# Performance work log

Measured on AMD Instinct MI355X. Metric: run time of the kernel, lower is better.

The kernel has to match this reference:

```python
import jax, jax.numpy as jnp
import numpy as np

B, C, P, NG, NCLS, HID, N, IMG = 2, 256, 7, 2, 81, 1024, 512, 800
STRIDES = [4, 8, 16, 32]
SCALE = 56.0  # roi_map_level_scale


def _roi_align(feat, rois, pooled, scale, ng):
    """torchvision-legacy (aligned=False) ROI Align. feat [B,C,H,W], rois [N,5]."""
    Bf, Cf, H, W = feat.shape
    ft = jnp.transpose(feat, (0, 2, 3, 1))  # [B,H,W,C]
    b = rois[:, 0].astype(jnp.int32)
    x1, y1, x2, y2 = (rois[:, i] * scale for i in (1, 2, 3, 4))
    rw = jnp.maximum(x2 - x1, 1.0)
    rh = jnp.maximum(y2 - y1, 1.0)
    # sample grid per output bin: ng points per axis, centered in sub-bins
    g = (jnp.arange(pooled)[:, None] + (jnp.arange(ng)[None, :] + 0.5) / ng).reshape(-1)  # [P*ng]
    ys = y1[:, None] + g[None, :] * (rh / pooled)[:, None]  # [N,S]
    xs = x1[:, None] + g[None, :] * (rw / pooled)[:, None]

    def axis(coord, size):
        valid = (coord >= -1.0) & (coord <= size)
        c = jnp.clip(coord, 0.0, size - 1)
        lo = jnp.floor(c).astype(jnp.int32)
        hi = jnp.minimum(lo + 1, size - 1)
        return valid, lo, hi, c - lo

    vy, ylo, yhi, fy = axis(ys, H)
    vx, xlo, xhi, fx = axis(xs, W)
    bb = b[:, None, None]

    def gather(yi, xi):
        return ft[bb, yi[:, :, None], xi[:, None, :], :]  # [N,S,S,C]

    wy = fy[:, :, None, None]
    wx = fx[:, None, :, None]
    val = ((1 - wy) * (1 - wx) * gather(ylo, xlo) + (1 - wy) * wx * gather(ylo, xhi)
           + wy * (1 - wx) * gather(yhi, xlo) + wy * wx * gather(yhi, xhi))
    val = jnp.where((vy[:, :, None] & vx[:, None, :])[..., None], val, 0.0)
    val = val.reshape(-1, pooled, ng, pooled, ng, Cf).mean(axis=(2, 4))  # [N,P,P,C]
    return jnp.transpose(val, (0, 3, 1, 2))  # [N,C,P,P]


def setup_inputs() -> dict:
    key = jax.random.key(0)
    ks = jax.random.split(key, 16)
    feats = {}
    for i, s in enumerate(STRIDES):
        hw = IMG // s
        feats[f"p{i+2}"] = jax.random.normal(ks[i], (B, C, hw, hw), jnp.float32)
    # realistic proposals: batch idx + boxes with sizes 16..512 px
    bidx = jax.random.randint(ks[4], (N,), 0, B).astype(jnp.float32)
    sw = 2.0 ** jax.random.uniform(ks[5], (N,), minval=4.0, maxval=9.0)
    sh = 2.0 ** jax.random.uniform(ks[6], (N,), minval=4.0, maxval=9.0)
    x1 = jax.random.uniform(ks[7], (N,)) * (IMG - sw)
    y1 = jax.random.uniform(ks[8], (N,)) * (IMG - sh)
    rois = jnp.stack([bidx, x1, y1, x1 + sw - 1, y1 + sh - 1], axis=1)
    D = C * P * P
    inp = dict(feats, rois=rois,
               w1=0.01 * jax.random.normal(ks[9], (HID, D), jnp.float32),
               b1=jnp.zeros((HID,), jnp.float32),
               w2=0.01 * jax.random.normal(ks[10], (HID, HID), jnp.float32),
               b2=jnp.zeros((HID,), jnp.float32),
               w_cls=0.01 * jax.random.normal(ks[11], (NCLS, HID), jnp.float32),
               b_cls=jnp.zeros((NCLS,), jnp.float32),
               w_reg=0.001 * jax.random.normal(ks[12], (NCLS * 4, HID), jnp.float32),
               b_reg=jnp.zeros((NCLS * 4,), jnp.float32))
    return inp


def reference(p2, p3, p4, p5, rois, w1, b1, w2, b2, w_cls, b_cls, w_reg, b_reg):
    feats = [p2, p3, p4, p5]
    # FPN level assignment (same math as torch: log2(sqrt(hw)/scale + 1e-6), floor, clamp)
    rh = rois[:, 4] - rois[:, 2] + 1
    rw = rois[:, 3] - rois[:, 1] + 1
    levels = jnp.clip(jnp.floor(jnp.log2(jnp.sqrt(rh * rw) / SCALE + 1e-6)), 0, 3).astype(jnp.int32)
    # dispatch: compute each ROI on its assigned level (masked combine == gather/sort-scatter)
    pooled = jnp.zeros((rois.shape[0], C, P, P), rois.dtype)
    for l, feat in enumerate(feats):
        pl = _roi_align(feat, rois, P, 1.0 / STRIDES[l], NG)
        pooled = pooled + jnp.where((levels == l)[:, None, None, None], pl, 0.0)
    x = pooled.reshape(pooled.shape[0], -1)  # [N, C*P*P]
    x = jax.nn.relu(x @ w1.T + b1)
    x = jax.nn.relu(x @ w2.T + b2)
    x_cls = x @ w_cls.T + b_cls
    x_reg = x @ w_reg.T + b_reg  # TEST mode, not class-agnostic: no gather
    cls_probs = jax.nn.softmax(x_cls, axis=1)
    rois_out = rois.reshape(B, -1, 5)
    cls_probs = cls_probs.reshape(B, rois_out.shape[1], -1)
    bbox_preds = x_reg.reshape(B, rois_out.shape[1], -1)
    return rois_out, cls_probs, bbox_preds
```

## Files before the change

### kernel.cpp

```cpp
#include <hip/hip_runtime.h>
#include <hip/hip_bf16.h>
#include <math.h>

#define NROI   512
#define CCH    256
#define POOLP  7
#define DDIM   12544
#define HIDN   1024
#define NCLS   81
#define NREG   324
#define NHEAD  512
#define OUT_ROIS   2560
#define OUT_CLS    (512*81)

typedef __attribute__((ext_vector_type(4))) float f32x4;
typedef __attribute__((ext_vector_type(8))) short bf16x8;

static __device__ __forceinline__ unsigned short f2bf(float x) {
    __hip_bfloat16 h = __float2bfloat16(x);
    return *reinterpret_cast<unsigned short*>(&h);
}
static __device__ __forceinline__ float bf2f(unsigned short u) {
    unsigned int b = ((unsigned int)u) << 16;
    return *reinterpret_cast<float*>(&b);
}

#define PP_B0 10
#define PP_B1 (PP_B0 + 1280)
#define PP_B2 (PP_B1 + 1024)
#define PP_B3 (PP_B2 + 1024)
#define PP_B4 (PP_B3 + 1024)
#define PP_B5 (PP_B4 + 13296)
__global__ __launch_bounds__(256) void preprocess_k(
        const float* __restrict__ rois, const float* __restrict__ w1,
        const float* __restrict__ w2, const float* __restrict__ wc,
        const float* __restrict__ wr,
        const float* __restrict__ p2, const float* __restrict__ p3,
        const float* __restrict__ p4, const float* __restrict__ p5,
        float* __restrict__ out, float* __restrict__ accz,
        unsigned short* __restrict__ w1b, unsigned short* __restrict__ w2b,
        unsigned short* __restrict__ whd,
        unsigned short* __restrict__ f0, unsigned short* __restrict__ f1,
        unsigned short* __restrict__ f2, unsigned short* __restrict__ f3) {
    __shared__ unsigned short sm[49 * 258];
    int bid = blockIdx.x, t = threadIdx.x;

    if (bid < PP_B0) {
        int i = bid * 256 + t;
        if (i < OUT_ROIS) out[i] = rois[i];
    } else if (bid < PP_B1) {
        int i = (bid - PP_B0) * 256 + t;
        ((float4*)accz)[i] = make_float4(0.f, 0.f, 0.f, 0.f);
    } else if (bid < PP_B2) {
        int i = (bid - PP_B1) * 256 + t;
        float4 v = ((const float4*)w2)[i];
        ushort4 o;
        o.x = f2bf(v.x); o.y = f2bf(v.y); o.z = f2bf(v.z); o.w = f2bf(v.w);
        ((ushort4*)w2b)[i] = o;
    } else if (bid < PP_B3) {
        int i2 = (bid - PP_B2) * 256 + t;
        int r = i2 >> 9, c = (i2 & 511) << 1;
        float v0, v1;
        if (r < NCLS)             { v0 = wc[r * HIDN + c]; v1 = wc[r * HIDN + c + 1]; }
        else if (r < NCLS + NREG) { v0 = wr[(r - NCLS) * HIDN + c]; v1 = wr[(r - NCLS) * HIDN + c + 1]; }
        else                      { v0 = 0.f; v1 = 0.f; }
        ((unsigned int*)whd)[i2] = (unsigned int)f2bf(v0) | ((unsigned int)f2bf(v1) << 16);
    } else if (bid < PP_B4) {
        int n = bid - PP_B3;
        const float* src = w1 + (size_t)n * DDIM;
        for (int k = t; k < DDIM; k += 256) {
            int c = k / 49;
            int s = k - c * 49;
            sm[s * 258 + c] = f2bf(src[k]);
        }
        __syncthreads();
        unsigned int* dst = (unsigned int*)(w1b + (size_t)n * DDIM);
        for (int j2 = t; j2 < DDIM / 2; j2 += 256) {
            int s = j2 >> 7, c2 = (j2 & 127) << 1;
            dst[j2] = sm[s * 258 + c2] | ((unsigned int)sm[s * 258 + c2 + 1] << 16);
        }
    } else {
        int j  = bid - PP_B4;
        int xb = j % 1662;
        int q  = j / 1662;
        int c0 = (q & 3) * 64;
        int b  = q >> 2;
        const float* in; unsigned short* op; int S, base;
        if (xb < 1250)      { in = p2; op = f0; S = 40000; base = 0; }
        else if (xb < 1563) { in = p3; op = f1; S = 10000; base = 1250; }
        else if (xb < 1642) { in = p4; op = f2; S = 2500;  base = 1563; }
        else                { in = p5; op = f3; S = 625;   base = 1642; }
        int s0 = (xb - base) * 32;
        {
            int sL = t & 31, cq = t >> 5;
            const float* src = in + ((size_t)b * CCH + c0 + cq * 8) * S + s0 + sL;
            bool ok = (s0 + sL) < S;
#pragma unroll
            for (int jj = 0; jj < 8; jj++)
                sm[sL * 66 + cq * 8 + jj] = ok ? f2bf(src[(size_t)jj * S]) : (unsigned short)0;
        }
        __syncthreads();
        {
            int c2 = t & 31, sq = t >> 5;
#pragma unroll
            for (int i = 0; i < 4; i++) {
                int s = sq * 4 + i;
                if (s0 + s < S) {
                    unsigned int v = sm[s * 66 + c2 * 2]
                                   | ((unsigned int)sm[s * 66 + c2 * 2 + 1] << 16);
                    ((unsigned int*)(op + ((size_t)b * S + s0 + s) * CCH + c0))[c2] = v;
                }
            }
        }
    }
}

__global__ __launch_bounds__(256) void roi_align_k(const unsigned short* __restrict__ f0,
                                                   const unsigned short* __restrict__ f1,
                                                   const unsigned short* __restrict__ f2,
                                                   const unsigned short* __restrict__ f3,
                                                   const float* __restrict__ rois,
                                                   unsigned short* __restrict__ xpool) {
    __shared__ float s_f[16];
    __shared__ int   s_lo[16], s_hi[16], s_v[16];

    int py = blockIdx.x, r = blockIdx.y, t = threadIdx.x;

    float r0  = rois[r * 5 + 0];
    float rx1 = rois[r * 5 + 1], ry1 = rois[r * 5 + 2];
    float rx2 = rois[r * 5 + 3], ry2 = rois[r * 5 + 4];
    int b = (int)r0;

    float aw = rx2 - rx1 + 1.f, ah = ry2 - ry1 + 1.f;
    float lvf = floorf(log2f(sqrtf(ah * aw) / 56.f + 1e-6f));
    int lv = (int)fminf(fmaxf(lvf, 0.f), 3.f);

    const unsigned short* F = (lv == 0) ? f0 : (lv == 1) ? f1 : (lv == 2) ? f2 : f3;
    int HW      = (lv == 0) ? 200 : (lv == 1) ? 100 : (lv == 2) ? 50 : 25;
    float scale = (lv == 0) ? 0.25f : (lv == 1) ? 0.125f : (lv == 2) ? 0.0625f : 0.03125f;

    float x1 = rx1 * scale, yy1 = ry1 * scale;
    float x2 = rx2 * scale, yy2 = ry2 * scale;
    float rw = fmaxf(x2 - x1, 1.f), rh = fmaxf(yy2 - yy1, 1.f);

    if (t < 16) {
        bool isY = t < 2;
        float coord;
        if (isY) {
            float g = (float)py + ((float)t + 0.5f) * 0.5f;
            coord = yy1 + g * (rh * (1.f / 7.f));
        } else {
            int j = t - 2;
            float g = (float)(j >> 1) + ((float)(j & 1) + 0.5f) * 0.5f;
            coord = x1 + g * (rw * (1.f / 7.f));
        }
        int vld = (coord >= -1.f && coord <= (float)HW) ? 1 : 0;
        float c = fminf(fmaxf(coord, 0.f), (float)(HW - 1));
        int lo  = (int)floorf(c);
        int hi  = min(lo + 1, HW - 1);
        s_v[t] = vld; s_lo[t] = lo; s_hi[t] = hi; s_f[t] = c - (float)lo;
    }
    __syncthreads();

    const unsigned short* Fb = F + ((size_t)b * HW * HW) * CCH + t;
    size_t obase = (size_t)r * DDIM + py * 7 * 256 + t;

    for (int px = 0; px < POOLP; px++) {
        float acc = 0.f;
#pragma unroll
        for (int s = 0; s < 4; s++) {
            int iy = s >> 1;
            int ix = px * 2 + (s & 1);
            int vy = s_v[iy], vx = s_v[2 + ix];
            if (vy & vx) {
                float fy = s_f[iy], fx = s_f[2 + ix];
                int ylo = s_lo[iy], yhi = s_hi[iy];
                int xlo = s_lo[2 + ix], xhi = s_hi[2 + ix];
                float v00 = bf2f(Fb[((size_t)ylo * HW + xlo) * CCH]);
                float v01 = bf2f(Fb[((size_t)ylo * HW + xhi) * CCH]);
                float v10 = bf2f(Fb[((size_t)yhi * HW + xlo) * CCH]);
                float v11 = bf2f(Fb[((size_t)yhi * HW + xhi) * CCH]);
                acc += (1.f - fy) * ((1.f - fx) * v00 + fx * v01)
                     + fy * ((1.f - fx) * v10 + fx * v11);
            }
        }
        xpool[obase + px * 256] = f2bf(acc * 0.25f);
    }
}

__global__ __launch_bounds__(256) void roi_align_nchw_k(const float* __restrict__ f0,
                                                        const float* __restrict__ f1,
                                                        const float* __restrict__ f2,
                                                        const float* __restrict__ f3,
                                                        const float* __restrict__ rois,
                                                        unsigned short* __restrict__ xpool) {
    __shared__ float s_f[16];
    __shared__ int   s_lo[16], s_hi[16], s_v[16];
    int py = blockIdx.x, r = blockIdx.y, t = threadIdx.x;
    float r0  = rois[r * 5 + 0];
    float rx1 = rois[r * 5 + 1], ry1 = rois[r * 5 + 2];
    float rx2 = rois[r * 5 + 3], ry2 = rois[r * 5 + 4];
    int b = (int)r0;
    float aw = rx2 - rx1 + 1.f, ah = ry2 - ry1 + 1.f;
    float lvf = floorf(log2f(sqrtf(ah * aw) / 56.f + 1e-6f));
    int lv = (int)fminf(fmaxf(lvf, 0.f), 3.f);
    const float* F = (lv == 0) ? f0 : (lv == 1) ? f1 : (lv == 2) ? f2 : f3;
    int HW      = (lv == 0) ? 200 : (lv == 1) ? 100 : (lv == 2) ? 50 : 25;
    float scale = (lv == 0) ? 0.25f : (lv == 1) ? 0.125f : (lv == 2) ? 0.0625f : 0.03125f;
    float x1 = rx1 * scale, yy1 = ry1 * scale;
    float x2 = rx2 * scale, yy2 = ry2 * scale;
    float rw = fmaxf(x2 - x1, 1.f), rh = fmaxf(yy2 - yy1, 1.f);
    if (t < 16) {
        bool isY = t < 2;
        float coord;
        if (isY) {
            float g = (float)py + ((float)t + 0.5f) * 0.5f;
            coord = yy1 + g * (rh * (1.f / 7.f));
        } else {
            int j = t - 2;
            float g = (float)(j >> 1) + ((float)(j & 1) + 0.5f) * 0.5f;
            coord = x1 + g * (rw * (1.f / 7.f));
        }
        int vld = (coord >= -1.f && coord <= (float)HW) ? 1 : 0;
        float c = fminf(fmaxf(coord, 0.f), (float)(HW - 1));
        int lo  = (int)floorf(c);
        int hi  = min(lo + 1, HW - 1);
        s_v[t] = vld; s_lo[t] = lo; s_hi[t] = hi; s_f[t] = c - (float)lo;
    }
    __syncthreads();
    const float* Fb = F + ((size_t)b * CCH + t) * HW * HW;
    size_t obase = (size_t)r * DDIM + py * 7 * 256 + t;
    for (int px = 0; px < POOLP; px++) {
        float acc = 0.f;
#pragma unroll
        for (int s = 0; s < 4; s++) {
            int iy = s >> 1, ix = px * 2 + (s & 1);
            int vy = s_v[iy], vx = s_v[2 + ix];
            if (vy & vx) {
                float fy = s_f[iy], fx = s_f[2 + ix];
                int ylo = s_lo[iy], yhi = s_hi[iy];
                int xlo = s_lo[2 + ix], xhi = s_hi[2 + ix];
                float v00 = Fb[(size_t)ylo * HW + xlo];
                float v01 = Fb[(size_t)ylo * HW + xhi];
                float v10 = Fb[(size_t)yhi * HW + xlo];
                float v11 = Fb[(size_t)yhi * HW + xhi];
                acc += (1.f - fy) * ((1.f - fx) * v00 + fx * v01)
                     + fy * ((1.f - fx) * v10 + fx * v11);
            }
        }
        xpool[obase + px * 256] = f2bf(acc * 0.25f);
    }
}

__global__ __launch_bounds__(256) void gemm_bf16_k(const unsigned short* __restrict__ A,
                                                   const unsigned short* __restrict__ W,
                                                   float* __restrict__ Cacc,
                                                   int M, int N, int K, int kchunk) {
    __shared__ __align__(16) unsigned short As[2][8][64][8];
    __shared__ __align__(16) unsigned short Ws[2][8][64][8];

    int t = threadIdx.x;
    int lane = t & 63, wid = t >> 6;
    int m0 = blockIdx.y * 64, n0 = blockIdx.x * 64;
    int k0 = blockIdx.z * kchunk;
    int wm = (wid >> 1) * 32, wn = (wid & 1) * 32;
    int fr = lane & 15, kg = lane >> 4;
    int nsteps = kchunk >> 6;

    f32x4 acc[2][2] = {};

    const unsigned short* Arow = A + (size_t)(m0 + lane) * K;
    const unsigned short* Wrow = W + (size_t)(n0 + lane) * K;

    auto stage = [&](int buf, int kb) {
#pragma unroll
        for (int i = 0; i < 2; i++) {
            int c = wid * 2 + i;
            __builtin_amdgcn_global_load_lds(
                (const __attribute__((address_space(1))) void*)(Arow + kb + c * 8),
                (__attribute__((address_space(3))) void*)(&As[buf][c][0][0]), 16, 0, 0);
            __builtin_amdgcn_global_load_lds(
                (const __attribute__((address_space(1))) void*)(Wrow + kb + c * 8),
                (__attribute__((address_space(3))) void*)(&Ws[buf][c][0][0]), 16, 0, 0);
        }
    };

    stage(0, k0);
    __syncthreads();
    int cur = 0;
    for (int tt = 0; tt < nsteps; ++tt) {
        if (tt + 1 < nsteps) stage(cur ^ 1, k0 + (tt + 1) * 64);
#pragma unroll
        for (int h = 0; h < 2; h++) {
            bf16x8 a0 = *(const bf16x8*)(&As[cur][h * 4 + kg][wm + fr][0]);
            bf16x8 a1 = *(const bf16x8*)(&As[cur][h * 4 + kg][wm + 16 + fr][0]);
            bf16x8 b0 = *(const bf16x8*)(&Ws[cur][h * 4 + kg][wn + fr][0]);
            bf16x8 b1 = *(const bf16x8*)(&Ws[cur][h * 4 + kg][wn + 16 + fr][0]);
            acc[0][0] = __builtin_amdgcn_mfma_f32_16x16x32_bf16(a0, b0, acc[0][0], 0, 0, 0);
            acc[0][1] = __builtin_amdgcn_mfma_f32_16x16x32_bf16(a0, b1, acc[0][1], 0, 0, 0);
            acc[1][0] = __builtin_amdgcn_mfma_f32_16x16x32_bf16(a1, b0, acc[1][0], 0, 0, 0);
            acc[1][1] = __builtin_amdgcn_mfma_f32_16x16x32_bf16(a1, b1, acc[1][1], 0, 0, 0);
        }
        __syncthreads();
        cur ^= 1;
    }

    int row = m0 + wm + (lane >> 4) * 4;
    int col = n0 + wn + fr;
#pragma unroll
    for (int fm = 0; fm < 2; fm++)
#pragma unroll
        for (int fn = 0; fn < 2; fn++)
#pragma unroll
            for (int r = 0; r < 4; r++)
                atomicAdd(&Cacc[(size_t)(row + fm * 16 + r) * N + col + fn * 16],
                          acc[fm][fn][r]);
}

__global__ __launch_bounds__(256) void gemm128_bf16_k(const unsigned short* __restrict__ A,
                                                      const unsigned short* __restrict__ W,
                                                      float* __restrict__ Cacc,
                                                      int M, int N, int K, int kchunk) {
    __shared__ __align__(16) unsigned short As[2][8][128][8];
    __shared__ __align__(16) unsigned short Ws[2][8][128][8];

    int lin  = blockIdx.x;
    int nb   = (lin & 7) * 56 + (lin >> 3);
    int tile = nb / 14, bz = nb - tile * 14;
    int bx = tile & 7, by = tile >> 3;

    int t = threadIdx.x;
    int lane = t & 63, wid = t >> 6;
    int m0 = by * 128, n0 = bx * 128;
    int k0 = bz * kchunk;
    int wm = (wid >> 1) * 64, wn = (wid & 1) * 64;
    int fr = lane & 15, kg = lane >> 4;
    int nsteps = kchunk >> 6;

    f32x4 acc[4][4] = {};

    auto stage = [&](int buf, int kb) {
#pragma unroll
        for (int i = 0; i < 4; i++) {
            int c   = wid * 4 + i;
            int kgc = c >> 1;
            int r0w = (c & 1) * 64;
            __builtin_amdgcn_global_load_lds(
                (const __attribute__((address_space(1))) void*)
                    (A + (size_t)(m0 + r0w + lane) * K + kb + kgc * 8),
                (__attribute__((address_space(3))) void*)(&As[buf][kgc][r0w][0]), 16, 0, 0);
            __builtin_amdgcn_global_load_lds(
                (const __attribute__((address_space(1))) void*)
                    (W + (size_t)(n0 + r0w + lane) * K + kb + kgc * 8),
                (__attribute__((address_space(3))) void*)(&Ws[buf][kgc][r0w][0]), 16, 0, 0);
        }
    };

    stage(0, k0);
    __syncthreads();
    int cur = 0;
    for (int tt = 0; tt < nsteps; ++tt) {
        if (tt + 1 < nsteps) stage(cur ^ 1, k0 + (tt + 1) * 64);
#pragma unroll
        for (int h = 0; h < 2; h++) {
            bf16x8 av[4], bv[4];
#pragma unroll
            for (int f = 0; f < 4; f++) {
                av[f] = *(const bf16x8*)(&As[cur][h * 4 + kg][wm + f * 16 + fr][0]);
                bv[f] = *(const bf16x8*)(&Ws[cur][h * 4 + kg][wn + f * 16 + fr][0]);
            }
#pragma unroll
            for (int fm = 0; fm < 4; fm++)
#pragma unroll
                for (int fn = 0; fn < 4; fn++)
                    acc[fm][fn] = __builtin_amdgcn_mfma_f32_16x16x32_bf16(
                        av[fm], bv[fn], acc[fm][fn], 0, 0, 0);
        }
        __syncthreads();
        cur ^= 1;
    }

    int row = m0 + wm + (lane >> 4) * 4;
    int col = n0 + wn + fr;
#pragma unroll
    for (int fm = 0; fm < 4; fm++)
#pragma unroll
        for (int fn = 0; fn < 4; fn++)
#pragma unroll
            for (int r = 0; r < 4; r++)
                atomicAdd(&Cacc[(size_t)(row + fm * 16 + r) * N + col + fn * 16],
                          acc[fm][fn][r]);
}

__global__ __launch_bounds__(256) void fc_ep_k(const float* __restrict__ acc,
                                               const float* __restrict__ bias,
                                               unsigned short* __restrict__ dst, int MN) {
    int i = blockIdx.x * 256 + threadIdx.x;
    if (i >= MN) return;
    float s = fmaxf(acc[i] + bias[i & (HIDN - 1)], 0.f);
    dst[i] = f2bf(s);
}

__global__ void head_ep_k(const float* __restrict__ hf,
                          const float* __restrict__ bc,
                          const float* __restrict__ br,
                          float* __restrict__ out) {
    int r = blockIdx.x, l = threadIdx.x;
    const float* row = hf + (size_t)r * NHEAD;

    float* reg = out + OUT_ROIS + OUT_CLS + (size_t)r * NREG;
    for (int j = l; j < NREG; j += 64) reg[j] = row[NCLS + j] + br[j];

    float v0 = row[l] + bc[l];
    float v1 = (l + 64 < NCLS) ? row[l + 64] + bc[l + 64] : -INFINITY;
    float m = fmaxf(v0, v1);
#pragma unroll
    for (int o = 32; o; o >>= 1) m = fmaxf(m, __shfl_xor(m, o));
    float e0 = __expf(v0 - m);
    float e1 = (l + 64 < NCLS) ? __expf(v1 - m) : 0.f;
    float s = e0 + e1;
#pragma unroll
    for (int o = 32; o; o >>= 1) s += __shfl_xor(s, o);
    float inv = 1.f / s;
    float* cls = out + OUT_ROIS + (size_t)r * NCLS;
    cls[l] = e0 * inv;
    if (l + 64 < NCLS) cls[l + 64] = e1 * inv;
}

extern "C" void kernel_launch(void* const* d_in, const int* in_sizes, int n_in,
                              void* d_out, int out_size, void* d_ws, size_t ws_size,
                              hipStream_t stream) {
    const float* p2   = (const float*)d_in[0];
    const float* p3   = (const float*)d_in[1];
    const float* p4   = (const float*)d_in[2];
    const float* p5   = (const float*)d_in[3];
    const float* rois = (const float*)d_in[4];
    const float* w1   = (const float*)d_in[5];
    const float* b1   = (const float*)d_in[6];
    const float* w2   = (const float*)d_in[7];
    const float* b2   = (const float*)d_in[8];
    const float* wc   = (const float*)d_in[9];
    const float* bc   = (const float*)d_in[10];
    const float* wr   = (const float*)d_in[11];
    const float* br   = (const float*)d_in[12];

    float* out = (float*)d_out;

    const int KS1 = 14;

    char* p = (char*)d_ws;
    auto alloc = [&](size_t bytes) { char* r = p; p += (bytes + 255) & ~(size_t)255; return r; };
    unsigned short* xpool = (unsigned short*)alloc((size_t)NROI * DDIM * 2);
    unsigned short* y1b   = (unsigned short*)alloc((size_t)NROI * HIDN * 2);
    unsigned short* y2b   = (unsigned short*)alloc((size_t)NROI * HIDN * 2);
    unsigned short* w1b   = (unsigned short*)alloc((size_t)HIDN * DDIM * 2);
    unsigned short* w2b   = (unsigned short*)alloc((size_t)HIDN * HIDN * 2);
    unsigned short* whd   = (unsigned short*)alloc((size_t)NHEAD * HIDN * 2);
    float*          accz  = (float*)alloc((size_t)(NROI * HIDN * 2 + NROI * NHEAD) * 4);
    unsigned short* ft0 = (unsigned short*)alloc((size_t)2 * 40000 * CCH * 2);
    unsigned short* ft1 = (unsigned short*)alloc((size_t)2 * 10000 * CCH * 2);
    unsigned short* ft2 = (unsigned short*)alloc((size_t)2 * 2500 * CCH * 2);
    unsigned short* ft3 = (unsigned short*)alloc((size_t)2 * 625 * CCH * 2);
    bool nhwc = (size_t)(p - (char*)d_ws) <= ws_size;

    float* y1f = accz;
    float* y2f = accz + (size_t)NROI * HIDN;
    float* hf  = accz + (size_t)NROI * HIDN * 2;

    preprocess_k<<<nhwc ? PP_B5 : PP_B4, 256, 0, stream>>>(
        rois, w1, w2, wc, wr, p2, p3, p4, p5,
        out, accz, w1b, w2b, whd, ft0, ft1, ft2, ft3);

    if (nhwc) {
        roi_align_k<<<dim3(POOLP, NROI), 256, 0, stream>>>(ft0, ft1, ft2, ft3, rois, xpool);
    } else {
        roi_align_nchw_k<<<dim3(POOLP, NROI), 256, 0, stream>>>(p2, p3, p4, p5, rois, xpool);
    }

    gemm128_bf16_k<<<8 * 4 * KS1, 256, 0, stream>>>(
        xpool, w1b, y1f, NROI, HIDN, DDIM, DDIM / KS1);
    fc_ep_k<<<(NROI * HIDN + 255) / 256, 256, 0, stream>>>(y1f, b1, y1b, NROI * HIDN);

    gemm_bf16_k<<<dim3(HIDN / 64, NROI / 64, 2), 256, 0, stream>>>(
        y1b, w2b, y2f, NROI, HIDN, HIDN, HIDN / 2);
    fc_ep_k<<<(NROI * HIDN + 255) / 256, 256, 0, stream>>>(y2f, b2, y2b, NROI * HIDN);

    gemm_bf16_k<<<dim3(NHEAD / 64, NROI / 64, 4), 256, 0, stream>>>(
        y2b, whd, hf, NROI, NHEAD, HIDN, HIDN / 4);
    head_ep_k<<<NROI, 64, 0, stream>>>(hf, bc, br, out);
}
```

Baseline: 162.1 us.

## Replace split-K atomics with partial buffers and split preprocessing into dedicated kernels

The first FC GEMM now writes each K-split's partial tile with plain stores into a scratch area that reuses the ft0 feature buffer. The epilogue kernel sums the 14 partials and applies bias and ReLU, which removes millions of global float atomicAdds. In exchange it adds about 29 MB of extra write and read traffic. The monolithic preprocess kernel is split into three kernels: a small-copy/convert kernel, a w1 permute kernel, and a new 64x64-tile NCHW->NHWC bf16 transpose that uses float4 loads and wider stores. The zeroed accumulator region shrinks because y1 no longer needs zeroing.

Result: faster. 156.8 us (-3.3%).

```diff
diff --git a/kernel.cpp b/kernel.cpp
--- a/kernel.cpp
+++ b/kernel.cpp
@@ -25,92 +25,108 @@
     return *reinterpret_cast<float*>(&b);
 }
 
-#define PP_B0 10
-#define PP_B1 (PP_B0 + 1280)
-#define PP_B2 (PP_B1 + 1024)
-#define PP_B3 (PP_B2 + 1024)
-#define PP_B4 (PP_B3 + 1024)
-#define PP_B5 (PP_B4 + 13296)
-__global__ __launch_bounds__(256) void preprocess_k(
-        const float* __restrict__ rois, const float* __restrict__ w1,
-        const float* __restrict__ w2, const float* __restrict__ wc,
-        const float* __restrict__ wr,
-        const float* __restrict__ p2, const float* __restrict__ p3,
-        const float* __restrict__ p4, const float* __restrict__ p5,
-        float* __restrict__ out, float* __restrict__ accz,
-        unsigned short* __restrict__ w1b, unsigned short* __restrict__ w2b,
-        unsigned short* __restrict__ whd,
-        unsigned short* __restrict__ f0, unsigned short* __restrict__ f1,
-        unsigned short* __restrict__ f2, unsigned short* __restrict__ f3) {
-    __shared__ unsigned short sm[49 * 258];
+#define PS_B0 10
+#define PS_B1 (PS_B0 + 768)
+#define PS_B2 (PS_B1 + 1024)
+#define PS_B3 (PS_B2 + 1024)
+__global__ __launch_bounds__(256) void prep_small_k(const float* __restrict__ rois,
+                                                    const float* __restrict__ w2,
+                                                    const float* __restrict__ wc,
+                                                    const float* __restrict__ wr,
+                                                    float* __restrict__ out,
+                                                    float* __restrict__ accz,
+                                                    unsigned short* __restrict__ w2b,
+                                                    unsigned short* __restrict__ whd) {
     int bid = blockIdx.x, t = threadIdx.x;
-
-    if (bid < PP_B0) {
+    if (bid < PS_B0) {
         int i = bid * 256 + t;
         if (i < OUT_ROIS) out[i] = rois[i];
-    } else if (bid < PP_B1) {
-        int i = (bid - PP_B0) * 256 + t;
+    } else if (bid < PS_B1) {
+        int i = (bid - PS_B0) * 256 + t;
         ((float4*)accz)[i] = make_float4(0.f, 0.f, 0.f, 0.f);
-    } else if (bid < PP_B2) {
-        int i = (bid - PP_B1) * 256 + t;
+    } else if (bid < PS_B2) {
+        int i = (bid - PS_B1) * 256 + t;
         float4 v = ((const float4*)w2)[i];
         ushort4 o;
         o.x = f2bf(v.x); o.y = f2bf(v.y); o.z = f2bf(v.z); o.w = f2bf(v.w);
         ((ushort4*)w2b)[i] = o;
-    } else if (bid < PP_B3) {
-        int i2 = (bid - PP_B2) * 256 + t;
+    } else {
+        int i2 = (bid - PS_B2) * 256 + t;
         int r = i2 >> 9, c = (i2 & 511) << 1;
         float v0, v1;
         if (r < NCLS)             { v0 = wc[r * HIDN + c]; v1 = wc[r * HIDN + c + 1]; }
         else if (r < NCLS + NREG) { v0 = wr[(r - NCLS) * HIDN + c]; v1 = wr[(r - NCLS) * HIDN + c + 1]; }
         else                      { v0 = 0.f; v1 = 0.f; }
         ((unsigned int*)whd)[i2] = (unsigned int)f2bf(v0) | ((unsigned int)f2bf(v1) << 16);
-    } else if (bid < PP_B4) {
-        int n = bid - PP_B3;
-        const float* src = w1 + (size_t)n * DDIM;
-        for (int k = t; k < DDIM; k += 256) {
-            int c = k / 49;
-            int s = k - c * 49;
-            sm[s * 258 + c] = f2bf(src[k]);
-        }
-        __syncthreads();
-        unsigned int* dst = (unsigned int*)(w1b + (size_t)n * DDIM);
-        for (int j2 = t; j2 < DDIM / 2; j2 += 256) {
-            int s = j2 >> 7, c2 = (j2 & 127) << 1;
-            dst[j2] = sm[s * 258 + c2] | ((unsigned int)sm[s * 258 + c2 + 1] << 16);
-        }
-    } else {
-        int j  = bid - PP_B4;
-        int xb = j % 1662;
-        int q  = j / 1662;
-        int c0 = (q & 3) * 64;
-        int b  = q >> 2;
-        const float* in; unsigned short* op; int S, base;
-        if (xb < 1250)      { in = p2; op = f0; S = 40000; base = 0; }
-        else if (xb < 1563) { in = p3; op = f1; S = 10000; base = 1250; }
-        else if (xb < 1642) { in = p4; op = f2; S = 2500;  base = 1563; }
-        else                { in = p5; op = f3; S = 625;   base = 1642; }
-        int s0 = (xb - base) * 32;
-        {
-            int sL = t & 31, cq = t >> 5;
-            const float* src = in + ((size_t)b * CCH + c0 + cq * 8) * S + s0 + sL;
-            bool ok = (s0 + sL) < S;
-#pragma unroll
-            for (int jj = 0; jj < 8; jj++)
-                sm[sL * 66 + cq * 8 + jj] = ok ? f2bf(src[(size_t)jj * S]) : (unsigned short)0;
-        }
-        __syncthreads();
-        {
-            int c2 = t & 31, sq = t >> 5;
-#pragma unroll
-            for (int i = 0; i < 4; i++) {
-                int s = sq * 4 + i;
-                if (s0 + s < S) {
-                    unsigned int v = sm[s * 66 + c2 * 2]
-                                   | ((unsigned int)sm[s * 66 + c2 * 2 + 1] << 16);
-                    ((unsigned int*)(op + ((size_t)b * S + s0 + s) * CCH + c0))[c2] = v;
-                }
-            }
+    }
+}
+
+__global__ __launch_bounds__(256) void permute_w1_k(const float* __restrict__ w1,
+                                                    unsigned short* __restrict__ w1b) {
+    __shared__ unsigned short lw[49 * 258];
+    int n = blockIdx.x, t = threadIdx.x;
+    const float* src = w1 + (size_t)n * DDIM;
+    for (int k = t; k < DDIM; k += 256) {
+        int c = k / 49;
+        int s = k - c * 49;
+        lw[s * 258 + c] = f2bf(src[k]);
+    }
+    __syncthreads();
+    unsigned int* dst = (unsigned int*)(w1b + (size_t)n * DDIM);
+    for (int j2 = t; j2 < DDIM / 2; j2 += 256) {
+        int s = j2 >> 7, c2 = (j2 & 127) << 1;
+        dst[j2] = lw[s * 258 + c2] | ((unsigned int)lw[s * 258 + c2 + 1] << 16);
+    }
+}
+
+__global__ __launch_bounds__(256) void transpose_k(const float* __restrict__ p2,
+                                                   const float* __restrict__ p3,
+                                                   const float* __restrict__ p4,
+                                                   const float* __restrict__ p5,
+                                                   unsigned short* __restrict__ f0,
+                                                   unsigned short* __restrict__ f1,
+                                                   unsigned short* __restrict__ f2,
+                                                   unsigned short* __restrict__ f3) {
+    __shared__ float sm[64][65];
+    int xb = blockIdx.x;
+    const float* in; unsigned short* op; int S, base;
+    if (xb < 625)      { in = p2; op = f0; S = 40000; base = 0; }
+    else if (xb < 782) { in = p3; op = f1; S = 10000; base = 625; }
+    else if (xb < 822) { in = p4; op = f2; S = 2500;  base = 782; }
+    else               { in = p5; op = f3; S = 625;   base = 822; }
+    int s0 = (xb - base) * 64;
+    int c0 = blockIdx.y * 64;
+    int b  = blockIdx.z;
+    int t  = threadIdx.x;
+
+    int sL = (t & 15) * 4, cc0 = t >> 4;
+    bool vec = (s0 + 64 <= S) && ((S & 3) == 0);
+#pragma unroll
+    for (int i = 0; i < 4; i++) {
+        int cc = cc0 + i * 16;
+        const float* src = in + ((size_t)(b * CCH + c0 + cc)) * S + s0 + sL;
+        if (vec) {
+            float4 v = *(const float4*)src;
+            sm[sL + 0][cc] = v.x; sm[sL + 1][cc] = v.y;
+            sm[sL + 2][cc] = v.z; sm[sL + 3][cc] = v.w;
+        } else {
+#pragma unroll
+            for (int j = 0; j < 4; j++)
+                sm[sL + j][cc] = (s0 + sL + j < S) ? src[j] : 0.f;
+        }
+    }
+    __syncthreads();
+
+    int cq = (t & 15) * 4, sr = t >> 4;
+#pragma unroll
+    for (int i = 0; i < 4; i++) {
+        int s = sr + i * 16;
+        if (s0 + s < S) {
+            float a = sm[s][cq], bb = sm[s][cq + 1], c = sm[s][cq + 2], d = sm[s][cq + 3];
+            uint2 v;
+            v.x = (unsigned int)f2bf(a) | ((unsigned int)f2bf(bb) << 16);
+            v.y = (unsigned int)f2bf(c) | ((unsigned int)f2bf(d) << 16);
+            *(uint2*)(op + ((size_t)b * S + s0 + s) * CCH + c0 + cq) = v;
         }
     }
 }
@@ -319,7 +335,7 @@
 
 __global__ __launch_bounds__(256) void gemm128_bf16_k(const unsigned short* __restrict__ A,
                                                       const unsigned short* __restrict__ W,
-                                                      float* __restrict__ Cacc,
+                                                      float* __restrict__ Cp,
                                                       int M, int N, int K, int kchunk) {
     __shared__ __align__(16) unsigned short As[2][8][128][8];
     __shared__ __align__(16) unsigned short Ws[2][8][128][8];
@@ -380,6 +396,7 @@
         cur ^= 1;
     }
 
+    float* Cout = Cp + (size_t)bz * ((size_t)M * N);
     int row = m0 + wm + (lane >> 4) * 4;
     int col = n0 + wn + fr;
 #pragma unroll
@@ -388,16 +405,18 @@
         for (int fn = 0; fn < 4; fn++)
 #pragma unroll
             for (int r = 0; r < 4; r++)
-                atomicAdd(&Cacc[(size_t)(row + fm * 16 + r) * N + col + fn * 16],
-                          acc[fm][fn][r]);
-}
-
-__global__ __launch_bounds__(256) void fc_ep_k(const float* __restrict__ acc,
+                Cout[(size_t)(row + fm * 16 + r) * N + col + fn * 16] = acc[fm][fn][r];
+}
+
+__global__ __launch_bounds__(256) void fc_ep_k(const float* __restrict__ Cp,
                                                const float* __restrict__ bias,
-                                               unsigned short* __restrict__ dst, int MN) {
+                                               unsigned short* __restrict__ dst,
+                                               int MN, int ks) {
     int i = blockIdx.x * 256 + threadIdx.x;
     if (i >= MN) return;
-    float s = fmaxf(acc[i] + bias[i & (HIDN - 1)], 0.f);
+    float s = 0.f;
+    for (int p = 0; p < ks; p++) s += Cp[(size_t)p * MN + i];
+    s = fmaxf(s + bias[i & (HIDN - 1)], 0.f);
     dst[i] = f2bf(s);
 }
 
@@ -456,34 +475,35 @@
     unsigned short* w1b   = (unsigned short*)alloc((size_t)HIDN * DDIM * 2);
     unsigned short* w2b   = (unsigned short*)alloc((size_t)HIDN * HIDN * 2);
     unsigned short* whd   = (unsigned short*)alloc((size_t)NHEAD * HIDN * 2);
-    float*          accz  = (float*)alloc((size_t)(NROI * HIDN * 2 + NROI * NHEAD) * 4);
+    float*          accz  = (float*)alloc((size_t)(NROI * HIDN + NROI * NHEAD) * 4);
     unsigned short* ft0 = (unsigned short*)alloc((size_t)2 * 40000 * CCH * 2);
     unsigned short* ft1 = (unsigned short*)alloc((size_t)2 * 10000 * CCH * 2);
     unsigned short* ft2 = (unsigned short*)alloc((size_t)2 * 2500 * CCH * 2);
     unsigned short* ft3 = (unsigned short*)alloc((size_t)2 * 625 * CCH * 2);
     bool nhwc = (size_t)(p - (char*)d_ws) <= ws_size;
 
-    float* y1f = accz;
-    float* y2f = accz + (size_t)NROI * HIDN;
-    float* hf  = accz + (size_t)NROI * HIDN * 2;
-
-    preprocess_k<<<nhwc ? PP_B5 : PP_B4, 256, 0, stream>>>(
-        rois, w1, w2, wc, wr, p2, p3, p4, p5,
-        out, accz, w1b, w2b, whd, ft0, ft1, ft2, ft3);
+    float* y2f = accz;
+    float* hf  = accz + (size_t)NROI * HIDN;
+    float* part = (float*)ft0;
+
+    prep_small_k<<<PS_B3, 256, 0, stream>>>(rois, w2, wc, wr, out, accz, w2b, whd);
+    permute_w1_k<<<HIDN, 256, 0, stream>>>(w1, w1b);
 
     if (nhwc) {
+        transpose_k<<<dim3(832, 4, 2), 256, 0, stream>>>(p2, p3, p4, p5,
+                                                         ft0, ft1, ft2, ft3);
         roi_align_k<<<dim3(POOLP, NROI), 256, 0, stream>>>(ft0, ft1, ft2, ft3, rois, xpool);
     } else {
         roi_align_nchw_k<<<dim3(POOLP, NROI), 256, 0, stream>>>(p2, p3, p4, p5, rois, xpool);
     }
 
     gemm128_bf16_k<<<8 * 4 * KS1, 256, 0, stream>>>(
-        xpool, w1b, y1f, NROI, HIDN, DDIM, DDIM / KS1);
-    fc_ep_k<<<(NROI * HIDN + 255) / 256, 256, 0, stream>>>(y1f, b1, y1b, NROI * HIDN);
+        xpool, w1b, part, NROI, HIDN, DDIM, DDIM / KS1);
+    fc_ep_k<<<(NROI * HIDN + 255) / 256, 256, 0, stream>>>(part, b1, y1b, NROI * HIDN, KS1);
 
     gemm_bf16_k<<<dim3(HIDN / 64, NROI / 64, 2), 256, 0, stream>>>(
         y1b, w2b, y2f, NROI, HIDN, HIDN, HIDN / 2);
-    fc_ep_k<<<(NROI * HIDN + 255) / 256, 256, 0, stream>>>(y2f, b2, y2b, NROI * HIDN);
+    fc_ep_k<<<(NROI * HIDN + 255) / 256, 256, 0, stream>>>(y2f, b2, y2b, NROI * HIDN, 1);
 
     gemm_bf16_k<<<dim3(NHEAD / 64, NROI / 64, 4), 256, 0, stream>>>(
         y2b, whd, hf, NROI, NHEAD, HIDN, HIDN / 4);
```
